# Performance work log

Measured on AMD Instinct MI355X. Metric: run time of the kernel, lower is better.

The kernel has to match this reference:

```python
import jax, jax.numpy as jnp
import numpy as np
from jax import lax

NUM_EXPERT = 2   # top-k experts kept per image
N_EXPERTS = 4    # total experts


def setup_inputs() -> dict:
    key = jax.random.key(0)
    ks = jax.random.split(key, 4)
    B, C, H, W = 16, 64, 128, 128
    inputs = jax.random.normal(ks[0], (B, C, H, W), dtype=jnp.float32)
    k = jax.random.uniform(ks[1], (B, C, 1, 1), dtype=jnp.float32)
    gate_w = jax.random.normal(ks[2], (N_EXPERTS, C), dtype=jnp.float32) * (1.0 / np.sqrt(C))
    gate_b = jnp.zeros((N_EXPERTS,), dtype=jnp.float32)
    conv_w = jax.random.normal(ks[3], (N_EXPERTS, C, C, 3, 3), dtype=jnp.float32) * (1.0 / np.sqrt(C * 9))
    conv_b = jnp.zeros((N_EXPERTS, C), dtype=jnp.float32)
    return {"inputs": inputs, "k": k, "gate_w": gate_w, "gate_b": gate_b,
            "conv_w": conv_w, "conv_b": conv_b}


def _expert(x, k, w, b):
    # expert_i(x, k) = ReLU(Conv3x3_i(x) + b_i) * k   (FiLM-style conditioning)
    y = lax.conv_general_dilated(x, w, window_strides=(1, 1), padding='SAME',
                                 dimension_numbers=('NCHW', 'OIHW', 'NCHW'))
    return jax.nn.relu(y + b[None, :, None, None]) * k


def reference(inputs, k, gate_w, gate_b, conv_w, conv_b):
    B = inputs.shape[0]
    # gate: global average pool over HW, then linear C -> E
    pooled = inputs.mean(axis=(2, 3))                       # [B, C]
    logits = pooled @ gate_w.T + gate_b                     # [B, E]
    # softmax in float32 (matches F.softmax(..., dtype=torch.float))
    weights = jax.nn.softmax(logits.astype(jnp.float32), axis=1).astype(inputs.dtype)
    topk_w, topk_idx = lax.top_k(weights, NUM_EXPERT)       # [B, num_expert]
    # scatter top-k weights into a dense [B, E] mask (zeros elsewhere)
    exp_weights = jnp.zeros_like(weights).at[jnp.arange(B)[:, None], topk_idx].set(topk_w)
    # dense loop over ALL experts, weighted sum with mostly-zero weights
    out = inputs
    for i in range(N_EXPERTS):
        out = out + _expert(inputs, k, conv_w[i], conv_b[i]) * exp_weights[:, i, None, None, None]
    return out
```

## Files before the change

kernel.cpp:

```cpp
#include <hip/hip_runtime.h>

typedef __attribute__((ext_vector_type(8))) short bfrag8;
typedef __attribute__((ext_vector_type(4))) short bfrag4;
typedef __attribute__((ext_vector_type(16))) float f32x16;

#define B_ 16
#define C_ 64
#define H_ 128
#define W_ 128
#define E_ 4
#define HW_ (H_ * W_)

#define NSL 66
#define PLANE2 (NSL * 16)
#define ROWB2  (8 * PLANE2)
#define RG 8
#define NRS 6

#define WT_ELEMS (4 * 9 * 2 * 4 * 64 * 8)
#define OFF_POOL (WT_ELEMS * 2)
#define OFF_EW   (OFF_POOL + 1024 * 4)
#define WS_NEEDED ((size_t)(OFF_EW + 64 * 4))

#define FB_WT_OFF 0
#define FB_POOLED_OFF 147456
#define FB_EW_OFF 148480

__device__ inline unsigned short f2bf(float f) {
    unsigned u = __builtin_bit_cast(unsigned, f);
    unsigned r = u + 0x7FFFu + ((u >> 16) & 1u);
    return (unsigned short)(r >> 16);
}
__device__ inline float bf2f(unsigned short s) {
    return __builtin_bit_cast(float, (unsigned)s << 16);
}

__global__ __launch_bounds__(256) void pool_wcvt(const float* __restrict__ in,
                                                 const float* __restrict__ cw,
                                                 float* __restrict__ pooled,
                                                 unsigned short* __restrict__ wT2) {
    if (blockIdx.x < 576) {
        const int idx = blockIdx.x * 256 + threadIdx.x;
        const int j = idx & 7;
        const int l = (idx >> 3) & 63;
        const int f = idx >> 9;
        const int kb = f & 3;
        const int chh = (f >> 2) & 1;
        const int et = f >> 3;
        const int tap = et % 9;
        const int e = et / 9;
        const int co = chh * 32 + (l & 31);
        const int ci = kb * 16 + (l >> 5) * 8 + j;
        wT2[idx] = f2bf(cw[(((e * C_ + co) * C_ + ci) * 9) + tap]);
    }
    const int bc = blockIdx.x;
    const float* p = in + (size_t)bc * HW_;
    float s = 0.f;
    for (int i = threadIdx.x; i < HW_ / 4; i += 256) {
        float4 v = ((const float4*)p)[i];
        s += v.x + v.y + v.z + v.w;
    }
    for (int off = 32; off; off >>= 1) s += __shfl_down(s, off);
    __shared__ float red[4];
    const int lane = threadIdx.x & 63, wv = threadIdx.x >> 6;
    if (lane == 0) red[wv] = s;
    __syncthreads();
    if (threadIdx.x == 0)
        pooled[bc] = (red[0] + red[1] + red[2] + red[3]) * (1.0f / (float)HW_);
}

__global__ void gate_kernel(const float* __restrict__ pooled,
                            const float* __restrict__ gate_w,
                            const float* __restrict__ gate_b,
                            float* __restrict__ ew) {
    const int b = threadIdx.x;
    if (b >= B_) return;
    float lg[E_];
    for (int e = 0; e < E_; e++) {
        float s = gate_b[e];
        for (int c = 0; c < C_; c++) s += pooled[b * C_ + c] * gate_w[e * C_ + c];
        lg[e] = s;
    }
    float m = fmaxf(fmaxf(lg[0], lg[1]), fmaxf(lg[2], lg[3]));
    float ex[E_], sum = 0.f;
    for (int e = 0; e < E_; e++) { ex[e] = expf(lg[e] - m); sum += ex[e]; }
    for (int e = 0; e < E_; e++) ex[e] /= sum;
    int i1 = 0;
    for (int e = 1; e < E_; e++) if (ex[e] > ex[i1]) i1 = e;
    int i2 = -1;
    for (int e = 0; e < E_; e++) {
        if (e == i1) continue;
        if (i2 < 0 || ex[e] > ex[i2]) i2 = e;
    }
    for (int e = 0; e < E_; e++)
        ew[b * E_ + e] = (e == i1 || e == i2) ? ex[e] : 0.f;
}

__global__ __launch_bounds__(512, 2) void conv_2r(const float* __restrict__ in,
                                                  const float* __restrict__ kk,
                                                  const float* __restrict__ cb,
                                                  const float* __restrict__ pooled,
                                                  const float* __restrict__ gw,
                                                  const float* __restrict__ gb,
                                                  const unsigned short* __restrict__ wT2,
                                                  float* __restrict__ out) {
    const int raw = blockIdx.x;
    const int swz = (raw & 7) * 64 + (raw >> 3);
    const int b   = swz >> 5;
    const int pxh = (swz >> 4) & 1;
    const int h0  = (swz & 15) * RG;
    const int x0g = pxh * 64;

    const int tid = threadIdx.x;
    const int lane = tid & 63;
    const int wv = tid >> 6;
    const int ln = lane & 31;
    const int lh = lane >> 5;
    const int rh = wv >> 2;
    const int ch = (wv >> 1) & 1;
    const int pq = wv & 1;
    const int co0 = ch * 32;

    const int spx = tid & 63;
    const int scg = (tid >> 6) & 3;
    const int srow = tid >> 8;

    __shared__ __align__(16) char ring[NRS * ROWB2];
    __shared__ float sEW[E_];

    if (tid < 64) {
        const float p = pooled[b * C_ + lane];
        float part[E_];
#pragma unroll
        for (int e = 0; e < E_; e++) part[e] = p * gw[e * C_ + lane];
#pragma unroll
        for (int off = 32; off; off >>= 1)
#pragma unroll
            for (int e = 0; e < E_; e++) part[e] += __shfl_down(part[e], off);
        if (lane == 0) {
            float lg[E_];
#pragma unroll
            for (int e = 0; e < E_; e++) lg[e] = part[e] + gb[e];
            float m = fmaxf(fmaxf(lg[0], lg[1]), fmaxf(lg[2], lg[3]));
            float ex[E_], sum = 0.f;
#pragma unroll
            for (int e = 0; e < E_; e++) { ex[e] = __expf(lg[e] - m); sum += ex[e]; }
            const float inv = 1.0f / sum;
            int i1 = 0;
            for (int e = 1; e < E_; e++) if (ex[e] > ex[i1]) i1 = e;
            int i2 = -1;
            for (int e = 0; e < E_; e++) {
                if (e == i1) continue;
                if (i2 < 0 || ex[e] > ex[i2]) i2 = e;
            }
#pragma unroll
            for (int e = 0; e < E_; e++)
                sEW[e] = (e == i1 || e == i2) ? ex[e] * inv : 0.f;
        }
    }
    __syncthreads();

    int e0 = 0, e1 = 0; float w0 = 0.f, w1 = 0.f;
    {
        int found = 0;
        for (int e = 0; e < E_; e++) {
            float we = sEW[e];
            if (we != 0.f) {
                if (!found) { e0 = e; w0 = we; found = 1; }
                else        { e1 = e; w1 = we; }
            }
        }
        if (w1 == 0.f) e1 = e0;
    }

    const float* cb0 = cb + e0 * C_;
    const float* cb1 = cb + e1 * C_;
    const float* kkp = kk + b * C_;

    float pv[16], ph[8];
    auto STAGE = [&](int pr) {
        const int r = pr + srow;
        if ((unsigned)r < (unsigned)H_) {
            const float* src = in + ((size_t)(b * C_ + scg * 16) * H_ + r) * W_ + x0g + spx;
#pragma unroll
            for (int i = 0; i < 16; ++i) pv[i] = src[(size_t)i * HW_];
        } else {
#pragma unroll
            for (int i = 0; i < 16; ++i) pv[i] = 0.f;
        }
        if (tid < 32) {
            const int hp = tid & 1;
            const int cgh = (tid >> 1) & 7;
            const int hrow = tid >> 4;
            const int rr = pr + hrow;
            const int pg = hp ? (x0g + 64) : (x0g - 1);
            const bool ok = ((unsigned)rr < (unsigned)H_) && ((unsigned)pg < (unsigned)W_);
            const float* src = in + ((size_t)(b * C_ + cgh * 8) * H_ + (((unsigned)rr < (unsigned)H_) ? rr : 0)) * W_ + (ok ? pg : 0);
#pragma unroll
            for (int i = 0; i < 8; ++i) ph[i] = ok ? src[(size_t)i * HW_] : 0.f;
        }
    };
    auto COMMIT = [&](int sl0) {
        int sl = sl0 + srow; if (sl >= NRS) sl -= NRS;
        bfrag8 f0, f1;
#pragma unroll
        for (int j = 0; j < 8; ++j) {
            f0[j] = (short)f2bf(pv[j]);
            f1[j] = (short)f2bf(pv[8 + j]);
        }
        char* bp = ring + sl * ROWB2 + (spx + 1) * 16;
        *(bfrag8*)(bp + (scg * 2) * PLANE2) = f0;
        *(bfrag8*)(bp + (scg * 2 + 1) * PLANE2) = f1;
        if (tid < 32) {
            const int hp = tid & 1;
            const int cgh = (tid >> 1) & 7;
            const int hrow = tid >> 4;
            int slh = sl0 + hrow; if (slh >= NRS) slh -= NRS;
            bfrag8 g;
#pragma unroll
            for (int i = 0; i < 8; ++i) g[i] = (short)f2bf(ph[i]);
            *(bfrag8*)(ring + slh * ROWB2 + cgh * PLANE2 + (hp ? 65 : 0) * 16) = g;
        }
    };

    STAGE(h0 - 1); COMMIT(0);
    STAGE(h0 + 1); COMMIT(2);
    __syncthreads();

    const char* wb0 = (const char*)wT2 + (size_t)e0 * 73728 + ch * 4096 + lane * 16;
    const char* wb1 = (const char*)wT2 + (size_t)e1 * 73728 + ch * 4096 + lane * 16;

    for (int t = 0; t < RG / 2; ++t) {
        if (t + 1 < RG / 2) STAGE(h0 + 2 * t + 3);

        const int myloc = 2 * t + rh;

        f32x16 Ae0, Ae1;
#pragma unroll
        for (int i = 0; i < 16; ++i) { Ae0[i] = 0.f; Ae1[i] = 0.f; }

#pragma unroll 1
        for (int ky = 0; ky < 3; ++ky) {
            int u = myloc + ky; if (u >= NRS) u -= NRS;
            const char* rb = ring + u * ROWB2;
            const char* wk0 = wb0 + ky * 24576;
            const char* wk1 = wb1 + ky * 24576;
#pragma unroll 1
            for (int kx = 0; kx < 3; ++kx) {
#pragma unroll
                for (int kb = 0; kb < 4; ++kb) {
                    bfrag8 a0 = *(const bfrag8*)(wk0 + kx * 8192 + kb * 1024);
                    bfrag8 a1 = *(const bfrag8*)(wk1 + kx * 8192 + kb * 1024);
                    bfrag8 bb = *(const bfrag8*)(rb + (kb * 2 + lh) * PLANE2
                                                 + (pq * 32 + ln + kx) * 16);
                    Ae0 = __builtin_amdgcn_mfma_f32_32x32x16_bf16(a0, bb, Ae0, 0, 0, 0);
                    Ae1 = __builtin_amdgcn_mfma_f32_32x32x16_bf16(a1, bb, Ae1, 0, 0, 0);
                }
            }
        }

        if (t + 1 < RG / 2) {
            int sl0 = 2 * t + 4; if (sl0 >= NRS) sl0 -= NRS;
            COMMIT(sl0);
        }

        const int row = h0 + 2 * t + rh;
        int v = myloc + 1; if (v >= NRS) v -= NRS;
        const char* rm1 = ring + v * ROWB2 + (pq * 32 + ln + 1) * 16 + lh * 8;
        bfrag4 ra[4];
#pragma unroll
        for (int c = 0; c < 4; ++c)
            ra[c] = *(const bfrag4*)(rm1 + (ch * 4 + c) * PLANE2);
#pragma unroll
        for (int g = 0; g < 16; ++g) {
            const int r_ = g & 3, c_ = g >> 2;
            const int co = co0 + r_ + 8 * c_ + 4 * lh;
            const float kv = kkp[co];
            const size_t oi = ((size_t)(b * C_ + co) * H_ + row) * W_ + x0g + pq * 32 + ln;
            out[oi] = bf2f((unsigned short)ra[c_][r_])
                      + fmaxf(Ae0[g] + cb0[co], 0.f) * (kv * w0)
                      + fmaxf(Ae1[g] + cb1[co], 0.f) * (kv * w1);
        }

        __syncthreads();
    }
}

#define CHUNK 32

__global__ __launch_bounds__(256) void pool_kernel(const float* __restrict__ in,
                                                   float* __restrict__ pooled) {
    const int bc = blockIdx.x;
    const float* p = in + (size_t)bc * HW_;
    float s = 0.f;
    for (int i = threadIdx.x; i < HW_ / 4; i += 256) {
        float4 v = ((const float4*)p)[i];
        s += v.x + v.y + v.z + v.w;
    }
    for (int off = 32; off; off >>= 1) s += __shfl_down(s, off);
    __shared__ float red[4];
    const int lane = threadIdx.x & 63, wv = threadIdx.x >> 6;
    if (lane == 0) red[wv] = s;
    __syncthreads();
    if (threadIdx.x == 0)
        pooled[bc] = (red[0] + red[1] + red[2] + red[3]) * (1.0f / (float)HW_);
}

__global__ __launch_bounds__(256) void wtr_kernel(const float* __restrict__ cw,
                                                  float* __restrict__ wT) {
    const int idx = blockIdx.x * 256 + threadIdx.x;
    if (idx >= E_ * C_ * 9 * C_) return;
    const int co = idx & 63;
    const int t2 = idx >> 6;
    const int tap = t2 % 9;
    const int t3 = t2 / 9;
    const int ci = t3 & 63;
    const int e = t3 >> 6;
    wT[idx] = cw[(((e * C_ + co) * C_ + ci) * 9) + tap];
}

__global__ __launch_bounds__(512) void conv_fallback(const float* __restrict__ in,
                                                     const float* __restrict__ kk,
                                                     const float* __restrict__ wT,
                                                     const float* __restrict__ cb,
                                                     const float* __restrict__ ew,
                                                     float* __restrict__ out) {
    const int bid = blockIdx.x;
    const int b = bid / H_;
    const int h = bid % H_;
    const int tid = threadIdx.x;
    const int lane = tid & 63;
    const int wv = tid >> 6;
    const int x0 = wv * 16;

    __shared__ float sIn[CHUNK * 3 * W_];

    float w0 = 0.f, w1 = 0.f;
    int e0 = 0, e1 = 0;
    {
        float we[E_];
#pragma unroll
        for (int e = 0; e < E_; e++) we[e] = ew[b * E_ + e];
        int found = 0;
        for (int e = 0; e < E_; e++) {
            if (we[e] != 0.f) {
                if (!found) { e0 = e; w0 = we[e]; found = 1; }
                else        { e1 = e; w1 = we[e]; }
            }
        }
        if (w1 == 0.f) e1 = e0;
    }

    float acc0[16], acc1[16];
#pragma unroll
    for (int i = 0; i < 16; i++) { acc0[i] = 0.f; acc1[i] = 0.f; }

    for (int cblk = 0; cblk < C_ / CHUNK; cblk++) {
        const int cbase = cblk * CHUNK;
        __syncthreads();
        for (int f = tid; f < CHUNK * 3 * W_ / 4; f += 512) {
            const int fi = f * 4;
            const int ci = fi / (3 * W_);
            const int rem = fi - ci * 3 * W_;
            const int kyy = rem / W_;
            const int x = rem - kyy * W_;
            const int hh = h + kyy - 1;
            float4 v = make_float4(0.f, 0.f, 0.f, 0.f);
            if (hh >= 0 && hh < H_)
                v = *(const float4*)(in + ((size_t)(b * C_ + cbase + ci) * H_ + hh) * W_ + x);
            *(float4*)(sIn + fi) = v;
        }
        __syncthreads();

        const float* wp0 = wT + (size_t)((e0 * C_ + cbase) * 9) * C_ + lane;
        const float* wp1 = wT + (size_t)((e1 * C_ + cbase) * 9) * C_ + lane;
        for (int ci = 0; ci < CHUNK; ci++) {
            float wa[9], wb[9];
#pragma unroll
            for (int t = 0; t < 9; t++) {
                wa[t] = wp0[(ci * 9 + t) * C_];
                wb[t] = wp1[(ci * 9 + t) * C_];
            }
            const float* rowp = sIn + ci * 3 * W_;
#pragma unroll
            for (int kyy = 0; kyy < 3; kyy++) {
                float xin[18];
                const float* rp = rowp + kyy * W_ + x0;
                xin[0] = (x0 == 0) ? 0.f : rp[-1];
#pragma unroll
                for (int j = 0; j < 16; j += 4) {
                    float4 v = *(const float4*)(rp + j);
                    xin[1 + j] = v.x; xin[2 + j] = v.y; xin[3 + j] = v.z; xin[4 + j] = v.w;
                }
                xin[17] = (x0 + 16 >= W_) ? 0.f : rp[16];
                const int t0 = kyy * 3;
#pragma unroll
                for (int x = 0; x < 16; x++) {
                    acc0[x] += xin[x] * wa[t0] + xin[x + 1] * wa[t0 + 1] + xin[x + 2] * wa[t0 + 2];
                    acc1[x] += xin[x] * wb[t0] + xin[x + 1] * wb[t0 + 1] + xin[x + 2] * wb[t0 + 2];
                }
            }
        }
    }

    const float kv = kk[b * C_ + lane];
    const float b0v = cb[e0 * C_ + lane];
    const float b1v = cb[e1 * C_ + lane];
    const float kw0 = kv * w0, kw1 = kv * w1;
    const size_t obase = ((size_t)(b * C_ + lane) * H_ + h) * W_ + x0;
#pragma unroll
    for (int x = 0; x < 16; x += 4) {
        float4 iv = *(const float4*)(in + obase + x);
        float4 ov;
        ov.x = iv.x + fmaxf(acc0[x + 0] + b0v, 0.f) * kw0 + fmaxf(acc1[x + 0] + b1v, 0.f) * kw1;
        ov.y = iv.y + fmaxf(acc0[x + 1] + b0v, 0.f) * kw0 + fmaxf(acc1[x + 1] + b1v, 0.f) * kw1;
        ov.z = iv.z + fmaxf(acc0[x + 2] + b0v, 0.f) * kw0 + fmaxf(acc1[x + 2] + b1v, 0.f) * kw1;
        ov.w = iv.w + fmaxf(acc0[x + 3] + b0v, 0.f) * kw0 + fmaxf(acc1[x + 3] + b1v, 0.f) * kw1;
        *(float4*)(out + obase + x) = ov;
    }
}

extern "C" void kernel_launch(void* const* d_in, const int* in_sizes, int n_in,
                              void* d_out, int out_size, void* d_ws, size_t ws_size,
                              hipStream_t stream) {
    const float* inputs = (const float*)d_in[0];
    const float* k      = (const float*)d_in[1];
    const float* gate_w = (const float*)d_in[2];
    const float* gate_b = (const float*)d_in[3];
    const float* conv_w = (const float*)d_in[4];
    const float* conv_b = (const float*)d_in[5];
    float* out = (float*)d_out;
    char* wsb = (char*)d_ws;

    if (ws_size >= WS_NEEDED) {
        unsigned short* wT2 = (unsigned short*)wsb;
        float* pooled = (float*)(wsb + OFF_POOL);

        pool_wcvt<<<B_ * C_, 256, 0, stream>>>(inputs, conv_w, pooled, wT2);
        conv_2r<<<512, 512, 0, stream>>>(inputs, k, conv_b, pooled,
                                         gate_w, gate_b, wT2, out);
    } else {
        float* ws = (float*)d_ws;
        float* wTf    = ws + FB_WT_OFF;
        float* pooled = ws + FB_POOLED_OFF;
        float* ewbuf  = ws + FB_EW_OFF;

        pool_kernel<<<B_ * C_, 256, 0, stream>>>(inputs, pooled);
        gate_kernel<<<1, 64, 0, stream>>>(pooled, gate_w, gate_b, ewbuf);
        wtr_kernel<<<(E_ * C_ * 9 * C_ + 255) / 256, 256, 0, stream>>>(conv_w, wTf);
        conv_fallback<<<B_ * H_, 512, 0, stream>>>(inputs, k, wTf, conv_b, ewbuf, out);
    }
}
```

Baseline: 84.14 us.

## Halve conv block to 4 waves with 2x2 MFMA accumulator tiles per wave

The conv kernel drops from 512 to 256 threads. Each wave now covers both 32-pixel halves of its row strip, holding four 32x32 accumulators (two experts by two pixel halves), so every weight fragment loaded feeds two MFMAs instead of one. Input staging switches to float4 global loads, with each thread converting four pixels by eight channels into bf16 fragments. In exchange each wave needs more accumulator registers, the launch bound is 256 threads with 1 block, and the kb loop is no longer unrolled, which lowers wave-level parallelism and latency hiding.

```diff
diff --git a/kernel.cpp b/kernel.cpp
--- a/kernel.cpp
+++ b/kernel.cpp
@@ -96,7 +96,7 @@
         ew[b * E_ + e] = (e == i1 || e == i2) ? ex[e] : 0.f;
 }
 
-__global__ __launch_bounds__(512, 2) void conv_2r(const float* __restrict__ in,
+__global__ __launch_bounds__(256, 1) void conv_4a(const float* __restrict__ in,
                                                   const float* __restrict__ kk,
                                                   const float* __restrict__ cb,
                                                   const float* __restrict__ pooled,
@@ -116,14 +116,13 @@
     const int wv = tid >> 6;
     const int ln = lane & 31;
     const int lh = lane >> 5;
-    const int rh = wv >> 2;
-    const int ch = (wv >> 1) & 1;
-    const int pq = wv & 1;
+    const int rh = wv >> 1;
+    const int ch = wv & 1;
     const int co0 = ch * 32;
 
-    const int spx = tid & 63;
-    const int scg = (tid >> 6) & 3;
-    const int srow = tid >> 8;
+    const int sq   = tid & 15;
+    const int sc   = (tid >> 4) & 7;
+    const int srow = tid >> 7;
 
     __shared__ __align__(16) char ring[NRS * ROWB2];
     __shared__ float sEW[E_];
@@ -177,16 +176,19 @@
     const float* cb1 = cb + e1 * C_;
     const float* kkp = kk + b * C_;
 
-    float pv[16], ph[8];
+    float4 pv4[8];
+    float ph[8];
     auto STAGE = [&](int pr) {
         const int r = pr + srow;
         if ((unsigned)r < (unsigned)H_) {
-            const float* src = in + ((size_t)(b * C_ + scg * 16) * H_ + r) * W_ + x0g + spx;
-#pragma unroll
-            for (int i = 0; i < 16; ++i) pv[i] = src[(size_t)i * HW_];
+            const float* src = in + ((size_t)(b * C_ + sc * 8) * H_ + r) * W_ + x0g + sq * 4;
+#pragma unroll
+            for (int i = 0; i < 8; ++i)
+                pv4[i] = *(const float4*)(src + (size_t)i * HW_);
         } else {
-#pragma unroll
-            for (int i = 0; i < 16; ++i) pv[i] = 0.f;
+            const float4 z = make_float4(0.f, 0.f, 0.f, 0.f);
+#pragma unroll
+            for (int i = 0; i < 8; ++i) pv4[i] = z;
         }
         if (tid < 32) {
             const int hp = tid & 1;
@@ -202,15 +204,16 @@
     };
     auto COMMIT = [&](int sl0) {
         int sl = sl0 + srow; if (sl >= NRS) sl -= NRS;
-        bfrag8 f0, f1;
-#pragma unroll
-        for (int j = 0; j < 8; ++j) {
-            f0[j] = (short)f2bf(pv[j]);
-            f1[j] = (short)f2bf(pv[8 + j]);
-        }
-        char* bp = ring + sl * ROWB2 + (spx + 1) * 16;
-        *(bfrag8*)(bp + (scg * 2) * PLANE2) = f0;
-        *(bfrag8*)(bp + (scg * 2 + 1) * PLANE2) = f1;
+        char* bp = ring + sl * ROWB2 + sc * PLANE2;
+#pragma unroll
+        for (int p = 0; p < 4; ++p) {
+            bfrag8 f;
+            f[0] = (short)f2bf(pv4[0][p]); f[1] = (short)f2bf(pv4[1][p]);
+            f[2] = (short)f2bf(pv4[2][p]); f[3] = (short)f2bf(pv4[3][p]);
+            f[4] = (short)f2bf(pv4[4][p]); f[5] = (short)f2bf(pv4[5][p]);
+            f[6] = (short)f2bf(pv4[6][p]); f[7] = (short)f2bf(pv4[7][p]);
+            *(bfrag8*)(bp + (sq * 4 + p + 1) * 16) = f;
+        }
         if (tid < 32) {
             const int hp = tid & 1;
             const int cgh = (tid >> 1) & 7;
@@ -235,9 +238,9 @@
 
         const int myloc = 2 * t + rh;
 
-        f32x16 Ae0, Ae1;
-#pragma unroll
-        for (int i = 0; i < 16; ++i) { Ae0[i] = 0.f; Ae1[i] = 0.f; }
+        f32x16 A00, A01, A10, A11;
+#pragma unroll
+        for (int i = 0; i < 16; ++i) { A00[i] = 0.f; A01[i] = 0.f; A10[i] = 0.f; A11[i] = 0.f; }
 
 #pragma unroll 1
         for (int ky = 0; ky < 3; ++ky) {
@@ -247,14 +250,17 @@
             const char* wk1 = wb1 + ky * 24576;
 #pragma unroll 1
             for (int kx = 0; kx < 3; ++kx) {
-#pragma unroll
+#pragma unroll 1
                 for (int kb = 0; kb < 4; ++kb) {
                     bfrag8 a0 = *(const bfrag8*)(wk0 + kx * 8192 + kb * 1024);
                     bfrag8 a1 = *(const bfrag8*)(wk1 + kx * 8192 + kb * 1024);
-                    bfrag8 bb = *(const bfrag8*)(rb + (kb * 2 + lh) * PLANE2
-                                                 + (pq * 32 + ln + kx) * 16);
-                    Ae0 = __builtin_amdgcn_mfma_f32_32x32x16_bf16(a0, bb, Ae0, 0, 0, 0);
-                    Ae1 = __builtin_amdgcn_mfma_f32_32x32x16_bf16(a1, bb, Ae1, 0, 0, 0);
+                    const char* bp = rb + (kb * 2 + lh) * PLANE2 + (ln + kx) * 16;
+                    bfrag8 b0 = *(const bfrag8*)(bp);
+                    bfrag8 b1 = *(const bfrag8*)(bp + 512);
+                    A00 = __builtin_amdgcn_mfma_f32_32x32x16_bf16(a0, b0, A00, 0, 0, 0);
+                    A01 = __builtin_amdgcn_mfma_f32_32x32x16_bf16(a0, b1, A01, 0, 0, 0);
+                    A10 = __builtin_amdgcn_mfma_f32_32x32x16_bf16(a1, b0, A10, 0, 0, 0);
+                    A11 = __builtin_amdgcn_mfma_f32_32x32x16_bf16(a1, b1, A11, 0, 0, 0);
                 }
             }
         }
@@ -266,20 +272,27 @@
 
         const int row = h0 + 2 * t + rh;
         int v = myloc + 1; if (v >= NRS) v -= NRS;
-        const char* rm1 = ring + v * ROWB2 + (pq * 32 + ln + 1) * 16 + lh * 8;
-        bfrag4 ra[4];
-#pragma unroll
-        for (int c = 0; c < 4; ++c)
-            ra[c] = *(const bfrag4*)(rm1 + (ch * 4 + c) * PLANE2);
+        const char* rm1 = ring + v * ROWB2 + lh * 8;
+        bfrag4 ra0[4], ra1[4];
+#pragma unroll
+        for (int c = 0; c < 4; ++c) {
+            ra0[c] = *(const bfrag4*)(rm1 + (ch * 4 + c) * PLANE2 + (ln + 1) * 16);
+            ra1[c] = *(const bfrag4*)(rm1 + (ch * 4 + c) * PLANE2 + (ln + 33) * 16);
+        }
 #pragma unroll
         for (int g = 0; g < 16; ++g) {
             const int r_ = g & 3, c_ = g >> 2;
             const int co = co0 + r_ + 8 * c_ + 4 * lh;
             const float kv = kkp[co];
-            const size_t oi = ((size_t)(b * C_ + co) * H_ + row) * W_ + x0g + pq * 32 + ln;
-            out[oi] = bf2f((unsigned short)ra[c_][r_])
-                      + fmaxf(Ae0[g] + cb0[co], 0.f) * (kv * w0)
-                      + fmaxf(Ae1[g] + cb1[co], 0.f) * (kv * w1);
+            const float f0 = kv * w0, f1 = kv * w1;
+            const float b0v = cb0[co], b1v = cb1[co];
+            const size_t base = ((size_t)(b * C_ + co) * H_ + row) * W_ + x0g;
+            out[base + ln]      = bf2f((unsigned short)ra0[c_][r_])
+                                  + fmaxf(A00[g] + b0v, 0.f) * f0
+                                  + fmaxf(A10[g] + b1v, 0.f) * f1;
+            out[base + 32 + ln] = bf2f((unsigned short)ra1[c_][r_])
+                                  + fmaxf(A01[g] + b0v, 0.f) * f0
+                                  + fmaxf(A11[g] + b1v, 0.f) * f1;
         }
 
         __syncthreads();
@@ -437,7 +450,7 @@
         float* pooled = (float*)(wsb + OFF_POOL);
 
         pool_wcvt<<<B_ * C_, 256, 0, stream>>>(inputs, conv_w, pooled, wT2);
-        conv_2r<<<512, 512, 0, stream>>>(inputs, k, conv_b, pooled,
+        conv_4a<<<512, 256, 0, stream>>>(inputs, k, conv_b, pooled,
                                          gate_w, gate_b, wT2, out);
     } else {
         float* ws = (float*)d_ws;
```

New measurement: 136.6 us. 1.62x slower.
